# Kernel tuning notes

Hardware: AMD Instinct MI355X
Metric: run time of the kernel (lower is better)

Reference implementation:

```python
import jax, jax.numpy as jnp
import numpy as np

WINDOW = 512          # init window_size
OVERLAP = WINDOW // 4 # 128
FADE = OVERLAP // 2   # 64
ROPE_BASE = 10000.0


def _rope(x, pos):
    # x: (B,H,nw,W,D), pos: (nw,W) float
    D = x.shape[-1]
    inv_freq = 1.0 / (ROPE_BASE ** (jnp.arange(0, D, 2, dtype=jnp.float32) / D))
    ang = pos[..., None] * inv_freq                     # (nw,W,D/2)
    cos = jnp.concatenate([jnp.cos(ang), jnp.cos(ang)], -1)[None, None]  # (1,1,nw,W,D)
    sin = jnp.concatenate([jnp.sin(ang), jnp.sin(ang)], -1)[None, None]
    x1, x2 = x[..., : D // 2], x[..., D // 2 :]
    rot = jnp.concatenate([-x2, x1], -1)
    return x * cos + rot * sin


def setup_inputs() -> dict:
    key = jax.random.key(0)
    k1, k2, k3 = jax.random.split(key, 3)
    B, H, L, D = 2, 16, 8192, 64
    return {
        "query": jax.random.normal(k1, (B, H, L, D), jnp.float32),
        "key": jax.random.normal(k2, (B, H, L, D), jnp.float32),
        "value": jax.random.normal(k3, (B, H, L, D), jnp.float32),
        "position_ids": jnp.arange(L, dtype=jnp.int64),
    }


def reference(query, key, value, position_ids):
    B, H, L, D = query.shape
    nw = L // WINDOW
    qw = query.reshape(B, H, nw, WINDOW, D)
    kw = key.reshape(B, H, nw, WINDOW, D)
    vw = value.reshape(B, H, nw, WINDOW, D)
    pos = position_ids.reshape(nw, WINDOW).astype(jnp.float32)

    q = _rope(qw, pos)
    k = _rope(kw, pos)

    scores = jnp.einsum("bhnqd,bhnkd->bhnqk", q, k) / jnp.sqrt(jnp.float32(D))
    attn = jax.nn.softmax(scores, axis=-1)
    win_out = jnp.einsum("bhnqk,bhnkd->bhnqd", attn, vw)  # (B,H,nw,W,D)

    # overlap-fade blend weights per window (middle windows fade at edges;
    # first/last windows use full weight). out = win_out * w / (w + 1e-8).
    fade_in = jnp.linspace(0.0, 1.0, FADE)
    fade_out = jnp.linspace(1.0, 0.0, FADE)
    w_mid = jnp.concatenate([fade_in, jnp.ones(WINDOW - 2 * FADE), fade_out])
    w_edge = jnp.ones(WINDOW)
    idx = jnp.arange(nw)
    is_edge = (idx == 0) | (idx == nw - 1)
    w = jnp.where(is_edge[:, None], w_edge[None, :], w_mid[None, :])  # (nw,W)
    scale = (w / (w + 1e-8))[None, None, :, :, None]
    out = win_out * scale
    return out.reshape(B, H, L, D)
```

## Files before the change

kernel.cpp:

```cpp
#include <hip/hip_runtime.h>

typedef _Float16 half8 __attribute__((ext_vector_type(8)));
typedef _Float16 half4 __attribute__((ext_vector_type(4)));
typedef float floatx4 __attribute__((ext_vector_type(4)));

#define MFMA_F16 __builtin_amdgcn_mfma_f32_16x16x32_f16
#define FREQ (-0.41524101186092f)

__global__ __launch_bounds__(256) void swa3(
    const float* __restrict__ Q, const float* __restrict__ K,
    const float* __restrict__ V, const int* __restrict__ pid,
    float* __restrict__ Out)
{
    __shared__ __align__(16) _Float16 lq[64 * 72];
    __shared__ __align__(16) _Float16 lk[32 * 64];
    __shared__ __align__(16) _Float16 lvt[64 * 32];
    __shared__ __align__(16) _Float16 lp[4][16 * 40];

    const int bid   = blockIdx.x;
    const int half_ = (bid >> 3) & 1;
    const int win   = (bid & 7) | ((bid >> 4) << 3);
    const int n = win & 15, bh = win >> 4;
    const long long winrow = (long long)bh * 8192 + n * 512;
    const long long qbase  = winrow + half_ * 256;
    const float* Qb = Q + qbase * 64;
    const float* Kb = K + winrow * 64;
    const float* Vb = V + winrow * 64;
    float* Ob = Out + qbase * 64;
    const int pidq = n * 512 + half_ * 256;
    const int pidk = n * 512;

    const int tid = threadIdx.x, lane = tid & 63, wv = tid >> 6;
    const int l15 = lane & 15, quad = lane >> 4;
    const float CS = 0.125f * 1.44269504088896f;

    half8 qf[4][2];
    {
        const int rowl = tid >> 2;
        const int dq   = (tid & 3) * 8;
        float ifq[8];
        #pragma unroll
        for (int i = 0; i < 8; ++i) ifq[i] = __builtin_exp2f((float)(dq + i) * FREQ);
        for (int rnd = 0; rnd < 4; ++rnd) {
            const float* src = Qb + (rnd * 64 + rowl) * 64;
            float pos = (float)pid[pidq + rnd * 64 + rowl];
            float4 a0 = *(const float4*)(src + dq);
            float4 a1 = *(const float4*)(src + dq + 4);
            float4 b0 = *(const float4*)(src + 32 + dq);
            float4 b1 = *(const float4*)(src + 36 + dq);
            float lo[8] = {a0.x,a0.y,a0.z,a0.w,a1.x,a1.y,a1.z,a1.w};
            float hi[8] = {b0.x,b0.y,b0.z,b0.w,b1.x,b1.y,b1.z,b1.w};
            half8 wlo, whi;
            #pragma unroll
            for (int i = 0; i < 8; ++i) {
                float sn, cn;
                __sincosf(pos * ifq[i], &sn, &cn);
                wlo[i] = (_Float16)((lo[i] * cn - hi[i] * sn) * CS);
                whi[i] = (_Float16)((hi[i] * cn + lo[i] * sn) * CS);
            }
            if (rnd) __syncthreads();
            *(half8*)&lq[rowl * 72 + dq]      = wlo;
            *(half8*)&lq[rowl * 72 + 32 + dq] = whi;
            __syncthreads();
            if (wv == rnd) {
                #pragma unroll
                for (int rt = 0; rt < 4; ++rt) {
                    qf[rt][0] = *(const half8*)&lq[(rt * 16 + l15) * 72 + quad * 8];
                    qf[rt][1] = *(const half8*)&lq[(rt * 16 + l15) * 72 + 32 + quad * 8];
                }
            }
        }
    }

    floatx4 o[4][4], ol[4];
    #pragma unroll
    for (int rt = 0; rt < 4; ++rt) {
        ol[rt] = (floatx4){0.f, 0.f, 0.f, 0.f};
        #pragma unroll
        for (int vt = 0; vt < 4; ++vt) o[rt][vt] = (floatx4){0.f, 0.f, 0.f, 0.f};
    }
    half8 onesf;
    #pragma unroll
    for (int i = 0; i < 8; ++i) onesf[i] = (_Float16)1.0f;

    const int key = tid >> 3;
    const int d0  = (tid & 7) * 4;
    const int dv  = tid & 63;
    const int k8  = (tid >> 6) & 3;
    float if4[4];
    #pragma unroll
    for (int i = 0; i < 4; ++i) if4[i] = __builtin_exp2f((float)(d0 + i) * FREQ);
    const int klo_addr = key * 64 + (((d0 >> 3) ^ (key & 7)) * 8) + (d0 & 7);
    const int khi_addr = key * 64 + ((((d0 >> 3) + 4) ^ (key & 7)) * 8) + (d0 & 7);
    const int vst_addr = dv * 32 + (k8 ^ ((dv >> 1) & 3)) * 8;
    const int ksw0 = (quad ^ (l15 & 7)) * 8;
    const int ksw1 = ((quad + 4) ^ (l15 & 7)) * 8;
    const int vsw  = (quad ^ ((l15 >> 1) & 3)) * 8;

    float4 ka = *(const float4*)(Kb + key * 64 + d0);
    float4 kb2 = *(const float4*)(Kb + key * 64 + 32 + d0);
    float vr[8];
    #pragma unroll
    for (int i = 0; i < 8; ++i) vr[i] = Vb[(k8 * 8 + i) * 64 + dv];

    for (int kc = 0; kc < 16; ++kc) {
        float kpos = (float)pid[pidk + kc * 32 + key];
        half4 klo, khi;
        {
            float a[4] = {ka.x, ka.y, ka.z, ka.w};
            float b[4] = {kb2.x, kb2.y, kb2.z, kb2.w};
            #pragma unroll
            for (int i = 0; i < 4; ++i) {
                float sn, cn;
                __sincosf(kpos * if4[i], &sn, &cn);
                klo[i] = (_Float16)(a[i] * cn - b[i] * sn);
                khi[i] = (_Float16)(b[i] * cn + a[i] * sn);
            }
        }
        half8 vh;
        #pragma unroll
        for (int i = 0; i < 8; ++i) vh[i] = (_Float16)vr[i];

        __syncthreads();
        *(half4*)&lk[klo_addr] = klo;
        *(half4*)&lk[khi_addr] = khi;
        *(half8*)&lvt[vst_addr] = vh;
        __syncthreads();

        if (kc < 15) {
            const float* kn = Kb + (kc + 1) * 2048;
            const float* vn = Vb + (kc + 1) * 2048;
            ka  = *(const float4*)(kn + key * 64 + d0);
            kb2 = *(const float4*)(kn + key * 64 + 32 + d0);
            #pragma unroll
            for (int i = 0; i < 8; ++i) vr[i] = vn[(k8 * 8 + i) * 64 + dv];
        }

        half8 kf00 = *(const half8*)&lk[l15 * 64 + ksw0];
        half8 kf01 = *(const half8*)&lk[l15 * 64 + ksw1];
        half8 kf10 = *(const half8*)&lk[(16 + l15) * 64 + ksw0];
        half8 kf11 = *(const half8*)&lk[(16 + l15) * 64 + ksw1];
        half8 vf[4];
        #pragma unroll
        for (int vt = 0; vt < 4; ++vt)
            vf[vt] = *(const half8*)&lvt[(vt * 16 + l15) * 32 + vsw];

        #pragma unroll
        for (int rt = 0; rt < 4; ++rt) {
            floatx4 s0 = {0.f,0.f,0.f,0.f}, s1 = {0.f,0.f,0.f,0.f};
            s0 = MFMA_F16(qf[rt][0], kf00, s0, 0, 0, 0);
            s0 = MFMA_F16(qf[rt][1], kf01, s0, 0, 0, 0);
            s1 = MFMA_F16(qf[rt][0], kf10, s1, 0, 0, 0);
            s1 = MFMA_F16(qf[rt][1], kf11, s1, 0, 0, 0);

            #pragma unroll
            for (int r = 0; r < 4; ++r) {
                float p0 = __builtin_exp2f(s0[r]);
                float p1 = __builtin_exp2f(s1[r]);
                lp[wv][(quad * 4 + r) * 40 + l15]      = (_Float16)p0;
                lp[wv][(quad * 4 + r) * 40 + 16 + l15] = (_Float16)p1;
            }
            half8 pf = *(const half8*)&lp[wv][l15 * 40 + quad * 8];
            ol[rt] = MFMA_F16(pf, onesf, ol[rt], 0, 0, 0);
            #pragma unroll
            for (int vt = 0; vt < 4; ++vt)
                o[rt][vt] = MFMA_F16(pf, vf[vt], o[rt][vt], 0, 0, 0);
        }
    }

    #pragma unroll
    for (int rt = 0; rt < 4; ++rt) {
        #pragma unroll
        for (int r = 0; r < 4; ++r) {
            int rowl = wv * 64 + rt * 16 + quad * 4 + r;
            int j = half_ * 256 + rowl;
            float w;
            if (n == 0 || n == 15)  w = 1.0f;
            else if (j < 64)        w = (float)j * (1.0f / 63.0f);
            else if (j >= 448)      w = (float)(511 - j) * (1.0f / 63.0f);
            else                    w = 1.0f;
            float f = (w / (w + 1e-8f)) / ol[rt][r];
            #pragma unroll
            for (int vt = 0; vt < 4; ++vt)
                Ob[rowl * 64 + vt * 16 + l15] = o[rt][vt][r] * f;
        }
    }
}

extern "C" void kernel_launch(void* const* d_in, const int* in_sizes, int n_in,
                              void* d_out, int out_size, void* d_ws, size_t ws_size,
                              hipStream_t stream) {
    const float* q   = (const float*)d_in[0];
    const float* k   = (const float*)d_in[1];
    const float* v   = (const float*)d_in[2];
    const int*   pid = (const int*)d_in[3];
    float* out = (float*)d_out;
    (void)in_sizes; (void)n_in; (void)out_size; (void)d_ws; (void)ws_size;
    swa3<<<dim3(1024), dim3(256), 0, stream>>>(q, k, v, pid, out);
}
```

Measured before the change: 273.0 us.

## Use 512-thread blocks with fewer rows per wave and double-buffered K/V LDS

Doubles the block to 8 waves so each wave handles 32 query rows instead of 64, halving per-wave accumulator registers. K and V staging is split across more threads with smaller loads. The LDS tiles are double-buffered so one barrier per chunk is removed, and the position id load is prefetched. The intent is more waves in flight to hide latency and lower sync overhead, at the cost of more LDS per block and K/V staging that is shared across more threads.

```diff
diff --git a/kernel.cpp b/kernel.cpp
--- a/kernel.cpp
+++ b/kernel.cpp
@@ -2,20 +2,22 @@
 
 typedef _Float16 half8 __attribute__((ext_vector_type(8)));
 typedef _Float16 half4 __attribute__((ext_vector_type(4)));
+typedef _Float16 half2v __attribute__((ext_vector_type(2)));
 typedef float floatx4 __attribute__((ext_vector_type(4)));
+typedef float floatx2 __attribute__((ext_vector_type(2)));
 
 #define MFMA_F16 __builtin_amdgcn_mfma_f32_16x16x32_f16
 #define FREQ (-0.41524101186092f)
 
-__global__ __launch_bounds__(256) void swa3(
+__global__ __launch_bounds__(512, 4) void swa4(
     const float* __restrict__ Q, const float* __restrict__ K,
     const float* __restrict__ V, const int* __restrict__ pid,
     float* __restrict__ Out)
 {
-    __shared__ __align__(16) _Float16 lq[64 * 72];
-    __shared__ __align__(16) _Float16 lk[32 * 64];
-    __shared__ __align__(16) _Float16 lvt[64 * 32];
-    __shared__ __align__(16) _Float16 lp[4][16 * 40];
+    __shared__ __align__(16) _Float16 lq[128 * 72];
+    __shared__ __align__(16) _Float16 lk[2][32 * 64];
+    __shared__ __align__(16) _Float16 lvt[2][64 * 32];
+    __shared__ __align__(16) _Float16 lp[8][16 * 40];
 
     const int bid   = blockIdx.x;
     const int half_ = (bid >> 3) & 1;
@@ -31,19 +33,19 @@
     const int pidk = n * 512;
 
     const int tid = threadIdx.x, lane = tid & 63, wv = tid >> 6;
-    const int l15 = lane & 15, quad = lane >> 4;
+    const int l15 = lane & 15, quad = (lane >> 4) & 3;
     const float CS = 0.125f * 1.44269504088896f;
 
-    half8 qf[4][2];
+    half8 qf[2][2];
     {
         const int rowl = tid >> 2;
         const int dq   = (tid & 3) * 8;
         float ifq[8];
         #pragma unroll
         for (int i = 0; i < 8; ++i) ifq[i] = __builtin_exp2f((float)(dq + i) * FREQ);
-        for (int rnd = 0; rnd < 4; ++rnd) {
-            const float* src = Qb + (rnd * 64 + rowl) * 64;
-            float pos = (float)pid[pidq + rnd * 64 + rowl];
+        for (int rnd = 0; rnd < 2; ++rnd) {
+            const float* src = Qb + (rnd * 128 + rowl) * 64;
+            float pos = (float)pid[pidq + rnd * 128 + rowl];
             float4 a0 = *(const float4*)(src + dq);
             float4 a1 = *(const float4*)(src + dq + 4);
             float4 b0 = *(const float4*)(src + 32 + dq);
@@ -62,19 +64,20 @@
             *(half8*)&lq[rowl * 72 + dq]      = wlo;
             *(half8*)&lq[rowl * 72 + 32 + dq] = whi;
             __syncthreads();
-            if (wv == rnd) {
+            if ((wv >> 2) == rnd) {
+                const int rb = (wv & 3) * 32;
                 #pragma unroll
-                for (int rt = 0; rt < 4; ++rt) {
-                    qf[rt][0] = *(const half8*)&lq[(rt * 16 + l15) * 72 + quad * 8];
-                    qf[rt][1] = *(const half8*)&lq[(rt * 16 + l15) * 72 + 32 + quad * 8];
+                for (int rt = 0; rt < 2; ++rt) {
+                    qf[rt][0] = *(const half8*)&lq[(rb + rt * 16 + l15) * 72 + quad * 8];
+                    qf[rt][1] = *(const half8*)&lq[(rb + rt * 16 + l15) * 72 + 32 + quad * 8];
                 }
             }
         }
     }
 
-    floatx4 o[4][4], ol[4];
-    #pragma unroll
-    for (int rt = 0; rt < 4; ++rt) {
+    floatx4 o[2][4], ol[2];
+    #pragma unroll
+    for (int rt = 0; rt < 2; ++rt) {
         ol[rt] = (floatx4){0.f, 0.f, 0.f, 0.f};
         #pragma unroll
         for (int vt = 0; vt < 4; ++vt) o[rt][vt] = (floatx4){0.f, 0.f, 0.f, 0.f};
@@ -83,70 +86,72 @@
     #pragma unroll
     for (int i = 0; i < 8; ++i) onesf[i] = (_Float16)1.0f;
 
-    const int key = tid >> 3;
-    const int d0  = (tid & 7) * 4;
+    const int key = tid >> 4;
+    const int pr  = tid & 15;
     const int dv  = tid & 63;
-    const int k8  = (tid >> 6) & 3;
-    float if4[4];
-    #pragma unroll
-    for (int i = 0; i < 4; ++i) if4[i] = __builtin_exp2f((float)(d0 + i) * FREQ);
-    const int klo_addr = key * 64 + (((d0 >> 3) ^ (key & 7)) * 8) + (d0 & 7);
-    const int khi_addr = key * 64 + ((((d0 >> 3) + 4) ^ (key & 7)) * 8) + (d0 & 7);
-    const int vst_addr = dv * 32 + (k8 ^ ((dv >> 1) & 3)) * 8;
+    const int grp = tid >> 6;
+    float if2[2];
+    #pragma unroll
+    for (int i = 0; i < 2; ++i) if2[i] = __builtin_exp2f((float)(pr * 2 + i) * FREQ);
+    const int klo_addr = key * 64 + (((pr >> 2) ^ (key & 7)) * 8) + (pr & 3) * 2;
+    const int khi_addr = key * 64 + ((((pr >> 2) + 4) ^ (key & 7)) * 8) + (pr & 3) * 2;
+    const int vst_addr = dv * 32 + (((grp >> 1) ^ ((dv >> 1) & 3)) * 8) + (grp & 1) * 4;
     const int ksw0 = (quad ^ (l15 & 7)) * 8;
     const int ksw1 = ((quad + 4) ^ (l15 & 7)) * 8;
     const int vsw  = (quad ^ ((l15 >> 1) & 3)) * 8;
 
-    float4 ka = *(const float4*)(Kb + key * 64 + d0);
-    float4 kb2 = *(const float4*)(Kb + key * 64 + 32 + d0);
-    float vr[8];
-    #pragma unroll
-    for (int i = 0; i < 8; ++i) vr[i] = Vb[(k8 * 8 + i) * 64 + dv];
+    floatx2 ka  = *(const floatx2*)(Kb + key * 64 + pr * 2);
+    floatx2 kb2 = *(const floatx2*)(Kb + key * 64 + 32 + pr * 2);
+    float vr[4];
+    #pragma unroll
+    for (int i = 0; i < 4; ++i) vr[i] = Vb[(grp * 4 + i) * 64 + dv];
+    int kp = pid[pidk + key];
 
     for (int kc = 0; kc < 16; ++kc) {
-        float kpos = (float)pid[pidk + kc * 32 + key];
-        half4 klo, khi;
+        const int cur = kc & 1;
+        float kpos = (float)kp;
+        half2v klo, khi;
         {
-            float a[4] = {ka.x, ka.y, ka.z, ka.w};
-            float b[4] = {kb2.x, kb2.y, kb2.z, kb2.w};
-            #pragma unroll
-            for (int i = 0; i < 4; ++i) {
+            float a[2] = {ka.x, ka.y};
+            float b[2] = {kb2.x, kb2.y};
+            #pragma unroll
+            for (int i = 0; i < 2; ++i) {
                 float sn, cn;
-                __sincosf(kpos * if4[i], &sn, &cn);
+                __sincosf(kpos * if2[i], &sn, &cn);
                 klo[i] = (_Float16)(a[i] * cn - b[i] * sn);
                 khi[i] = (_Float16)(b[i] * cn + a[i] * sn);
             }
         }
-        half8 vh;
-        #pragma unroll
-        for (int i = 0; i < 8; ++i) vh[i] = (_Float16)vr[i];
-
-        __syncthreads();
-        *(half4*)&lk[klo_addr] = klo;
-        *(half4*)&lk[khi_addr] = khi;
-        *(half8*)&lvt[vst_addr] = vh;
+        half4 vh;
+        #pragma unroll
+        for (int i = 0; i < 4; ++i) vh[i] = (_Float16)vr[i];
+
+        *(half2v*)&lk[cur][klo_addr] = klo;
+        *(half2v*)&lk[cur][khi_addr] = khi;
+        *(half4*)&lvt[cur][vst_addr] = vh;
         __syncthreads();
 
         if (kc < 15) {
             const float* kn = Kb + (kc + 1) * 2048;
             const float* vn = Vb + (kc + 1) * 2048;
-            ka  = *(const float4*)(kn + key * 64 + d0);
-            kb2 = *(const float4*)(kn + key * 64 + 32 + d0);
-            #pragma unroll
-            for (int i = 0; i < 8; ++i) vr[i] = vn[(k8 * 8 + i) * 64 + dv];
-        }
-
-        half8 kf00 = *(const half8*)&lk[l15 * 64 + ksw0];
-        half8 kf01 = *(const half8*)&lk[l15 * 64 + ksw1];
-        half8 kf10 = *(const half8*)&lk[(16 + l15) * 64 + ksw0];
-        half8 kf11 = *(const half8*)&lk[(16 + l15) * 64 + ksw1];
+            ka  = *(const floatx2*)(kn + key * 64 + pr * 2);
+            kb2 = *(const floatx2*)(kn + key * 64 + 32 + pr * 2);
+            #pragma unroll
+            for (int i = 0; i < 4; ++i) vr[i] = vn[(grp * 4 + i) * 64 + dv];
+            kp = pid[pidk + (kc + 1) * 32 + key];
+        }
+
+        half8 kf00 = *(const half8*)&lk[cur][l15 * 64 + ksw0];
+        half8 kf01 = *(const half8*)&lk[cur][l15 * 64 + ksw1];
+        half8 kf10 = *(const half8*)&lk[cur][(16 + l15) * 64 + ksw0];
+        half8 kf11 = *(const half8*)&lk[cur][(16 + l15) * 64 + ksw1];
         half8 vf[4];
         #pragma unroll
         for (int vt = 0; vt < 4; ++vt)
-            vf[vt] = *(const half8*)&lvt[(vt * 16 + l15) * 32 + vsw];
-
-        #pragma unroll
-        for (int rt = 0; rt < 4; ++rt) {
+            vf[vt] = *(const half8*)&lvt[cur][(vt * 16 + l15) * 32 + vsw];
+
+        #pragma unroll
+        for (int rt = 0; rt < 2; ++rt) {
             floatx4 s0 = {0.f,0.f,0.f,0.f}, s1 = {0.f,0.f,0.f,0.f};
             s0 = MFMA_F16(qf[rt][0], kf00, s0, 0, 0, 0);
             s0 = MFMA_F16(qf[rt][1], kf01, s0, 0, 0, 0);
@@ -169,10 +174,10 @@
     }
 
     #pragma unroll
-    for (int rt = 0; rt < 4; ++rt) {
+    for (int rt = 0; rt < 2; ++rt) {
         #pragma unroll
         for (int r = 0; r < 4; ++r) {
-            int rowl = wv * 64 + rt * 16 + quad * 4 + r;
+            int rowl = wv * 32 + rt * 16 + quad * 4 + r;
             int j = half_ * 256 + rowl;
             float w;
             if (n == 0 || n == 15)  w = 1.0f;
@@ -196,5 +201,5 @@
     const int*   pid = (const int*)d_in[3];
     float* out = (float*)d_out;
     (void)in_sizes; (void)n_in; (void)out_size; (void)d_ws; (void)ws_size;
-    swa3<<<dim3(1024), dim3(256), 0, stream>>>(q, k, v, pid, out);
+    swa4<<<dim3(1024), dim3(512), 0, stream>>>(q, k, v, pid, out);
 }
```

Measured after the change: 238.1 us. 12.8% less time.
